# Kernel optimization log

Hardware: AMD Instinct MI355X
Metric: run time of the kernel (lower is better)

## Reference

```python
import jax, jax.numpy as jnp
import numpy as np

B, N, C, H, W = 4, 5, 64, 96, 288
DOWNSAMPLE_RATE = 4
DISCRETE_RATIO = 0.4
DECAY_WEIGHTS = jax.nn.softmax(jnp.array([1.0, 0.5], dtype=jnp.float32))  # frame=1, decay=0.5


def _warp_one(img, theta):
    # img: (C,H,W), theta: (2,3). Matches F.affine_grid + F.grid_sample
    # (bilinear, zeros padding, align_corners=True).
    c, h, w = img.shape
    xs = jnp.linspace(-1.0, 1.0, w, dtype=img.dtype)
    ys = jnp.linspace(-1.0, 1.0, h, dtype=img.dtype)
    gy, gx = jnp.meshgrid(ys, xs, indexing='ij')
    base = jnp.stack([gx.ravel(), gy.ravel(), jnp.ones(h * w, img.dtype)], 0)  # (3, HW)
    g = theta @ base  # (2, HW) normalized coords
    px = (g[0] + 1.0) * 0.5 * (w - 1)
    py = (g[1] + 1.0) * 0.5 * (h - 1)
    x0 = jnp.floor(px); y0 = jnp.floor(py)
    wx = px - x0; wy = py - y0
    def tap(yy, xx):
        yi = jnp.clip(yy, 0, h - 1).astype(jnp.int32)
        xi = jnp.clip(xx, 0, w - 1).astype(jnp.int32)
        valid = ((yy >= 0) & (yy <= h - 1) & (xx >= 0) & (xx <= w - 1)).astype(img.dtype)
        return img[:, yi, xi] * valid  # (C, HW)
    out = (tap(y0, x0) * (1 - wx) * (1 - wy)
           + tap(y0, x0 + 1) * wx * (1 - wy)
           + tap(y0 + 1, x0) * (1 - wx) * wy
           + tap(y0 + 1, x0 + 1) * wx * wy)
    return out.reshape(c, h, w)


def _frame_score(hist, mlp_w, mlp_b):
    # hist: (B,N,C,H,W) -> per-pixel ego-vs-neighbor attention score (B,N,1,H,W).
    b, n, c, h, w = hist.shape
    node = hist.reshape(b, n, c, h * w).transpose(0, 3, 1, 2)  # (B, P, N, C)
    ego = node[:, :, 0]          # (B, P, C)
    neigh = node[:, :, 1:]       # (B, P, N-1, C)
    # Query rows are all the repeated ego vector -> one row suffices (identical math).
    s = jnp.einsum('bpc,bpkc->bpk', ego, neigh) / jnp.sqrt(jnp.asarray(c, hist.dtype))
    attn = jax.nn.softmax(s, axis=-1)
    ctx = jnp.einsum('bpk,bpkc->bpc', attn, neigh)
    sc = jax.nn.sigmoid(ctx @ mlp_w.T + mlp_b)                   # (B, P, 1)
    sc = jnp.broadcast_to(sc[:, :, None, :], (b, h * w, n - 1, 1))
    ego_sc = jnp.ones((b, h * w, 1, 1), hist.dtype)
    overall = jnp.concatenate([ego_sc, sc], axis=2)              # (B, P, N, 1)
    return overall.transpose(0, 2, 3, 1).reshape(b, n, 1, h, w)


def _forward(x0, x1, pairwise_t_matrix, mlp_w, mlp_b):
    x0g = x0.reshape(B, N, C, H, W)
    x1g = x1.reshape(B, N, C, H, W)

    # --- TemporalSampling: weighted per-frame scores, threshold, 3x3 max-pool ---
    conf = DECAY_WEIGHTS[0] * _frame_score(x0g, mlp_w, mlp_b) \
         + DECAY_WEIGHTS[1] * _frame_score(x1g, mlp_w, mlp_b)      # (B,N,1,H,W)
    mask = jnp.where(conf > 0.5, jnp.float32(1.0), jnp.float32(0.0))
    mask = jax.lax.reduce_window(mask, -jnp.inf, jax.lax.max,
                                 (1, 1, 1, 3, 3), (1, 1, 1, 1, 1), 'SAME')
    x = x0g * mask  # broadcast over C

    # --- normalize pairwise transform to 2x3 affine matrices ---
    t = pairwise_t_matrix[:, :, :, jnp.array([0, 1])][:, :, :, :, jnp.array([0, 1, 3])]  # (B,L,L,2,3)
    t = t.at[..., 0, 1].mul(H / W)
    t = t.at[..., 1, 0].mul(W / H)
    t = t.at[..., 0, 2].set(t[..., 0, 2] / (DOWNSAMPLE_RATE * DISCRETE_RATIO * W) * 2)
    t = t.at[..., 1, 2].set(t[..., 1, 2] / (DOWNSAMPLE_RATE * DISCRETE_RATIO * H) * 2)
    theta = t[:, 0]  # (B,N,2,3): warp each cav into ego frame

    # --- per-agent warp ---
    warped = jax.vmap(jax.vmap(_warp_one))(x, theta)  # (B,N,C,H,W)

    # --- AttenFusion: per-pixel NxN attention, keep ego row ---
    nf = warped.reshape(B, N, C, H * W).transpose(0, 3, 1, 2)  # (B, P, N, C)
    s = jnp.einsum('bpc,bpkc->bpk', nf[:, :, 0], nf) / jnp.sqrt(jnp.asarray(C, nf.dtype))
    attn = jax.nn.softmax(s, axis=-1)
    ctx = jnp.einsum('bpk,bpkc->bpc', attn, nf)                 # (B, P, C)
    x_fuse = ctx.transpose(0, 2, 1).reshape(B, C, H, W)
    return x_fuse


def setup_inputs() -> dict:
    key = jax.random.key(0)
    k0, k1, k2, k3 = jax.random.split(key, 4)
    x0 = jax.random.normal(k0, (B * N, C, H, W), dtype=jnp.float32)
    x1 = jax.random.normal(k1, (B * N, C, H, W), dtype=jnp.float32)
    eye = jnp.broadcast_to(jnp.eye(4, dtype=jnp.float32), (B, N, N, 4, 4))
    pairwise_t_matrix = eye + 0.01 * jax.random.normal(k2, (B, N, N, 4, 4), dtype=jnp.float32)
    mlp_w = 0.1 * jax.random.normal(k3, (1, C), dtype=jnp.float32)
    mlp_b = jnp.zeros((1,), dtype=jnp.float32)
    record_len = jnp.full((B,), N, dtype=jnp.int32)
    return {"x0": x0, "x1": x1, "pairwise_t_matrix": pairwise_t_matrix,
            "mlp_w": mlp_w, "mlp_b": mlp_b, "record_len": record_len}


def reference(x0, x1, pairwise_t_matrix, mlp_w, mlp_b, record_len):
    # record_len is uniform (=N) and only determines the static regrouping.
    return _forward(x0, x1, pairwise_t_matrix, mlp_w, mlp_b)
```

## Files before the change

kernel.cpp:

```cpp
#include <hip/hip_runtime.h>
#include <cmath>

#define BB 4
#define NN 5
#define CC 64
#define HH 96
#define WW 288
#define PP (HH*WW)
#define BP (BB*PP)
#define CP (CC*PP)
#define NCP (NN*CC*PP)


static __device__ __forceinline__ float sigmoidf_(float x) {
    return 1.0f / (1.0f + expf(-x));
}

static __device__ __forceinline__ void tap_setup(
    int b, int h, int w, const float* __restrict__ pmat,
    const float* __restrict__ pooled, int offs[NN][4], float wts[NN][4])
{
    float gx = -1.0f + 2.0f * (float)w / (float)(WW - 1);
    float gy = -1.0f + 2.0f * (float)h / (float)(HH - 1);
    #pragma unroll
    for (int n = 0; n < NN; n++) {
        const float* m = pmat + ((size_t)(b * NN + 0) * NN + n) * 16;
        float t00 = m[0];
        float t01 = m[1] * ((float)HH / (float)WW);
        float t02 = m[3] * (float)(2.0 / (4.0 * 0.4 * (double)WW));
        float t10 = m[4] * ((float)WW / (float)HH);
        float t11 = m[5];
        float t12 = m[7] * (float)(2.0 / (4.0 * 0.4 * (double)HH));

        float g0 = t00 * gx + t01 * gy + t02;
        float g1 = t10 * gx + t11 * gy + t12;
        float px = (g0 + 1.0f) * 0.5f * (float)(WW - 1);
        float py = (g1 + 1.0f) * 0.5f * (float)(HH - 1);
        float x0f = floorf(px), y0f = floorf(py);
        float wx = px - x0f, wy = py - y0f;
        float bw[4] = { (1.f - wx) * (1.f - wy), wx * (1.f - wy),
                        (1.f - wx) * wy,         wx * wy };
        #pragma unroll
        for (int t = 0; t < 4; t++) {
            float xx = (t & 1) ? (x0f + 1.0f) : x0f;
            float yy = (t >> 1) ? (y0f + 1.0f) : y0f;
            int xi = min(max((int)xx, 0), WW - 1);
            int yi = min(max((int)yy, 0), HH - 1);
            float valid = (yy >= 0.0f && yy <= (float)(HH - 1) &&
                           xx >= 0.0f && xx <= (float)(WW - 1)) ? 1.0f : 0.0f;
            float mk = (n == 0) ? 1.0f : pooled[b * PP + yi * WW + xi];
            offs[n][t] = yi * WW + xi;
            wts[n][t]  = bw[t] * valid * mk;
        }
    }
}

__global__ __launch_bounds__(256) void mask_part_kernel(
    const float* __restrict__ x0, const float* __restrict__ x1,
    const float* __restrict__ mlp_w, float* __restrict__ mpart)
{
    int idx = blockIdx.x * blockDim.x + threadIdx.x;
    int seg = blockIdx.y;
    int b = idx / PP;
    int p = idx - b * PP;
    const float* xt = (seg >> 2) ? x1 : x0;
    int c0 = (seg & 3) * 16;
    const float* base = xt + (size_t)b * NCP + p;

    float d0=0.f,d1=0.f,d2=0.f,d3=0.f, m0=0.f,m1=0.f,m2=0.f,m3=0.f;
    #pragma unroll 4
    for (int ci = 0; ci < 16; ci++) {
        int c = c0 + ci;
        const float* q = base + (size_t)c * PP;
        float e  = q[0];
        float wc = mlp_w[c];
        float v1 = q[(size_t)1 * CP];
        float v2 = q[(size_t)2 * CP];
        float v3 = q[(size_t)3 * CP];
        float v4 = q[(size_t)4 * CP];
        d0 += e * v1;  m0 += wc * v1;
        d1 += e * v2;  m1 += wc * v2;
        d2 += e * v3;  m2 += wc * v3;
        d3 += e * v4;  m3 += wc * v4;
    }
    float vals[8] = {d0,d1,d2,d3,m0,m1,m2,m3};
    #pragma unroll
    for (int j = 0; j < 8; j++)
        mpart[((size_t)seg * 8 + j) * BP + idx] = vals[j];
}

__global__ __launch_bounds__(256) void mask_comb_kernel(
    const float* __restrict__ mpart, const float* __restrict__ mlp_b,
    float* __restrict__ premask)
{
    int idx = blockIdx.x * blockDim.x + threadIdx.x;
    float bias = mlp_b[0];
    float scv[2];
    #pragma unroll
    for (int t = 0; t < 2; t++) {
        float d[4] = {0.f,0.f,0.f,0.f};
        float m[4] = {0.f,0.f,0.f,0.f};
        #pragma unroll
        for (int cs = 0; cs < 4; cs++) {
            int seg = t * 4 + cs;
            #pragma unroll
            for (int j = 0; j < 4; j++) {
                d[j] += mpart[((size_t)seg * 8 + j) * BP + idx];
                m[j] += mpart[((size_t)seg * 8 + 4 + j) * BP + idx];
            }
        }
        float s0 = d[0]*0.125f, s1 = d[1]*0.125f, s2 = d[2]*0.125f, s3 = d[3]*0.125f;
        float mx = fmaxf(fmaxf(s0, s1), fmaxf(s2, s3));
        float e0 = expf(s0-mx), e1 = expf(s1-mx), e2 = expf(s2-mx), e3 = expf(s3-mx);
        float inv = 1.0f / (e0+e1+e2+e3);
        float z = (e0*m[0] + e1*m[1] + e2*m[2] + e3*m[3]) * inv + bias;
        scv[t] = sigmoidf_(z);
    }
    const float W0 = 0.6224593312018546f, W1 = 0.3775406687981454f;
    float conf = W0 * scv[0] + W1 * scv[1];
    premask[idx] = (conf > 0.5f) ? 1.0f : 0.0f;
}

__global__ __launch_bounds__(256) void pool_kernel(
    const float* __restrict__ pre, float* __restrict__ pooled)
{
    int idx = blockIdx.x * blockDim.x + threadIdx.x;
    int b = idx / PP;
    int p = idx - b * PP;
    int h = p / WW;
    int w = p - h * WW;
    const float* pb = pre + (size_t)b * PP;
    float m = 0.0f;
    #pragma unroll
    for (int dy = -1; dy <= 1; dy++) {
        int y = h + dy;
        if (y < 0 || y >= HH) continue;
        #pragma unroll
        for (int dx = -1; dx <= 1; dx++) {
            int x = w + dx;
            if (x < 0 || x >= WW) continue;
            m = fmaxf(m, pb[y * WW + x]);
        }
    }
    pooled[idx] = m;
}

__global__ __launch_bounds__(256) void dot_part_kernel(
    const float* __restrict__ x0, const float* __restrict__ pmat,
    const float* __restrict__ pooled, float* __restrict__ dpart)
{
    int idx = blockIdx.x * blockDim.x + threadIdx.x;
    int seg = blockIdx.y;
    int b = idx / PP;
    int p = idx - b * PP;
    int h = p / WW;
    int w = p - h * WW;

    int offs[NN][4];
    float wts[NN][4];
    tap_setup(b, h, w, pmat, pooled, offs, wts);

    const float* base = x0 + (size_t)b * NCP;
    float dot[NN] = {0.f,0.f,0.f,0.f,0.f};
    #pragma unroll 4
    for (int ci = 0; ci < 16; ci++) {
        int c = seg * 16 + ci;
        float v[NN];
        #pragma unroll
        for (int n = 0; n < NN; n++) {
            const float* pl = base + ((size_t)n * CC + c) * PP;
            float acc = 0.f;
            #pragma unroll
            for (int t = 0; t < 4; t++)
                acc += wts[n][t] * pl[offs[n][t]];
            v[n] = acc;
        }
        #pragma unroll
        for (int n = 0; n < NN; n++)
            dot[n] += v[0] * v[n];
    }
    #pragma unroll
    for (int n = 0; n < NN; n++)
        dpart[((size_t)n * 4 + seg) * BP + idx] = dot[n];
}

__global__ __launch_bounds__(256) void attn_kernel(
    const float* __restrict__ dpart, const float* __restrict__ pmat,
    const float* __restrict__ pooled, float* __restrict__ aw,
    int* __restrict__ offout)
{
    int idx = blockIdx.x * blockDim.x + threadIdx.x;
    int b = idx / PP;
    int p = idx - b * PP;
    int h = p / WW;
    int w = p - h * WW;

    float dot[NN];
    #pragma unroll
    for (int n = 0; n < NN; n++) {
        float s = 0.f;
        #pragma unroll
        for (int seg = 0; seg < 4; seg++)
            s += dpart[((size_t)n * 4 + seg) * BP + idx];
        dot[n] = s;
    }
    float s[NN], attn[NN];
    float mx = -INFINITY;
    #pragma unroll
    for (int n = 0; n < NN; n++) { s[n] = dot[n] * 0.125f; mx = fmaxf(mx, s[n]); }
    float sum = 0.f;
    #pragma unroll
    for (int n = 0; n < NN; n++) { attn[n] = expf(s[n] - mx); sum += attn[n]; }
    float inv = 1.0f / sum;

    int offs[NN][4];
    float wts[NN][4];
    tap_setup(b, h, w, pmat, pooled, offs, wts);
    #pragma unroll
    for (int n = 0; n < NN; n++) {
        float a = attn[n] * inv;
        #pragma unroll
        for (int t = 0; t < 4; t++) {
            aw[((size_t)n * 4 + t) * BP + idx]     = a * wts[n][t];
            offout[((size_t)n * 4 + t) * BP + idx] = offs[n][t];
        }
    }
}

__global__ __launch_bounds__(256) void out_kernel(
    const float* __restrict__ x0, const float* __restrict__ aw,
    const int* __restrict__ offin, float* __restrict__ out)
{
    int idx = blockIdx.x * blockDim.x + threadIdx.x;
    int c0  = blockIdx.y * 4;
    int b = idx / PP;
    int p = idx - b * PP;

    float a[20];
    int   o[20];
    #pragma unroll
    for (int j = 0; j < 20; j++) {
        a[j] = aw[(size_t)j * BP + idx];
        o[j] = offin[(size_t)j * BP + idx];
    }

    const float* base = x0 + (size_t)b * NCP + (size_t)c0 * PP;
    float acc0 = 0.f, acc1 = 0.f, acc2 = 0.f, acc3 = 0.f;
    #pragma unroll
    for (int j = 0; j < 20; j++) {
        int n = j >> 2;
        const float* pl = base + (size_t)n * CP + o[j];
        float w = a[j];
        acc0 += w * pl[0];
        acc1 += w * pl[(size_t)1 * PP];
        acc2 += w * pl[(size_t)2 * PP];
        acc3 += w * pl[(size_t)3 * PP];
    }
    size_t ob = ((size_t)b * CC + c0) * PP + p;
    out[ob]                 = acc0;
    out[ob + (size_t)1*PP]  = acc1;
    out[ob + (size_t)2*PP]  = acc2;
    out[ob + (size_t)3*PP]  = acc3;
}

extern "C" void kernel_launch(void* const* d_in, const int* in_sizes, int n_in,
                              void* d_out, int out_size, void* d_ws, size_t ws_size,
                              hipStream_t stream) {
    const float* x0    = (const float*)d_in[0];
    float*       x1    = (float*)d_in[1];
    const float* pmat  = (const float*)d_in[2];
    const float* mlp_w = (const float*)d_in[3];
    const float* mlp_b = (const float*)d_in[4];
    float* out = (float*)d_out;

    float* mpart  = out;
    float* s_pre  = x1;
    float* s_pool = x1 + (size_t)1  * BP;
    float* s_dot  = x1 + (size_t)2  * BP;
    float* s_aw   = x1 + (size_t)22 * BP;
    int*   s_off  = (int*)(x1 + (size_t)42 * BP);

    dim3 blk(256);
    dim3 g1(BP / 256, 8);
    dim3 g2(BP / 256);
    dim3 gf1(BP / 256, 4);
    dim3 gf2(BP / 256, 16);

    mask_part_kernel<<<g1,  blk, 0, stream>>>(x0, x1, mlp_w, mpart);
    mask_comb_kernel<<<g2,  blk, 0, stream>>>(mpart, mlp_b, s_pre);
    pool_kernel     <<<g2,  blk, 0, stream>>>(s_pre, s_pool);
    dot_part_kernel <<<gf1, blk, 0, stream>>>(x0, pmat, s_pool, s_dot);
    attn_kernel     <<<g2,  blk, 0, stream>>>(s_dot, pmat, s_pool, s_aw, s_off);
    out_kernel      <<<gf2, blk, 0, stream>>>(x0, s_aw, s_off, out);
}
```

Before: 474.4 us.

## Materialize warped features once and vectorize all kernels with float4

Adds a warp kernel that computes the bilinear-sampled neighbor features once and stores them. The dot-product and output kernels then read this warped tensor with coalesced float4 loads, so they no longer redo the 20-tap gathers or read per-tap weight and offset arrays. All per-pixel kernels now handle four pixels per thread using float4. The cost is an extra full-size write and two reads of the warped tensor, and the input buffers x0 and x1 are now overwritten as scratch space.

```diff
diff --git a/kernel.cpp b/kernel.cpp
--- a/kernel.cpp
+++ b/kernel.cpp
@@ -10,34 +10,177 @@
 #define BP (BB*PP)
 #define CP (CC*PP)
 #define NCP (NN*CC*PP)
+#define QP (PP/4)
+#define BQ (BP/4)
+#define CPQ (CP/4)
+#define NCPQ (NCP/4)
 
 
 static __device__ __forceinline__ float sigmoidf_(float x) {
     return 1.0f / (1.0f + expf(-x));
 }
-
-static __device__ __forceinline__ void tap_setup(
-    int b, int h, int w, const float* __restrict__ pmat,
-    const float* __restrict__ pooled, int offs[NN][4], float wts[NN][4])
-{
-    float gx = -1.0f + 2.0f * (float)w / (float)(WW - 1);
+static __device__ __forceinline__ float4 f4zero() {
+    return make_float4(0.f, 0.f, 0.f, 0.f);
+}
+static __device__ __forceinline__ void fma4(float4& a, float s, const float4& v) {
+    a.x += s * v.x; a.y += s * v.y; a.z += s * v.z; a.w += s * v.w;
+}
+static __device__ __forceinline__ void fma44(float4& a, const float4& s, const float4& v) {
+    a.x += s.x * v.x; a.y += s.y * v.y; a.z += s.z * v.z; a.w += s.w * v.w;
+}
+
+static __device__ __forceinline__ void theta_load(
+    const float* __restrict__ pmat, int b, int n,
+    float& t00, float& t01, float& t02, float& t10, float& t11, float& t12)
+{
+    const float* m = pmat + ((size_t)(b * NN + 0) * NN + n) * 16;
+    t00 = m[0];
+    t01 = m[1] * ((float)HH / (float)WW);
+    t02 = m[3] * (float)(2.0 / (4.0 * 0.4 * (double)WW));
+    t10 = m[4] * ((float)WW / (float)HH);
+    t11 = m[5];
+    t12 = m[7] * (float)(2.0 / (4.0 * 0.4 * (double)HH));
+}
+
+__global__ __launch_bounds__(256) void mask_part_kernel(
+    const float4* __restrict__ x0, const float4* __restrict__ x1,
+    const float* __restrict__ mlp_w, float4* __restrict__ mpart)
+{
+    int q   = blockIdx.x * 256 + threadIdx.x;
+    int seg = blockIdx.y;
+    int b  = q / QP;
+    int qp = q - b * QP;
+    const float4* xt = (seg >= 4) ? x1 : x0;
+    int c0 = (seg & 3) * 16;
+    const float4* base = xt + (size_t)b * NCPQ + qp;
+
+    float4 d0 = f4zero(), d1 = f4zero(), d2 = f4zero(), d3 = f4zero();
+    float4 m0 = f4zero(), m1 = f4zero(), m2 = f4zero(), m3 = f4zero();
+    #pragma unroll 4
+    for (int ci = 0; ci < 16; ci++) {
+        int c = c0 + ci;
+        const float4* qq = base + (size_t)c * QP;
+        float4 e  = qq[0];
+        float  wc = mlp_w[c];
+        float4 v1 = qq[(size_t)1 * CPQ];
+        float4 v2 = qq[(size_t)2 * CPQ];
+        float4 v3 = qq[(size_t)3 * CPQ];
+        float4 v4 = qq[(size_t)4 * CPQ];
+        fma44(d0, e, v1);  fma4(m0, wc, v1);
+        fma44(d1, e, v2);  fma4(m1, wc, v2);
+        fma44(d2, e, v3);  fma4(m2, wc, v3);
+        fma44(d3, e, v4);  fma4(m3, wc, v4);
+    }
+    float4 vals[8] = {d0, d1, d2, d3, m0, m1, m2, m3};
+    #pragma unroll
+    for (int j = 0; j < 8; j++)
+        mpart[((size_t)seg * 8 + j) * BQ + q] = vals[j];
+}
+
+__global__ __launch_bounds__(256) void mask_comb_kernel(
+    const float4* mpart, const float* mlp_b, float4* premask)
+{
+    int q = blockIdx.x * 256 + threadIdx.x;
+    float bias = mlp_b[0];
+    float4 scv[2];
+    #pragma unroll
+    for (int t = 0; t < 2; t++) {
+        float4 d[4] = {f4zero(), f4zero(), f4zero(), f4zero()};
+        float4 m[4] = {f4zero(), f4zero(), f4zero(), f4zero()};
+        #pragma unroll
+        for (int cs = 0; cs < 4; cs++) {
+            int seg = t * 4 + cs;
+            #pragma unroll
+            for (int j = 0; j < 4; j++) {
+                float4 dv = mpart[((size_t)seg * 8 + j) * BQ + q];
+                float4 mv = mpart[((size_t)seg * 8 + 4 + j) * BQ + q];
+                d[j].x += dv.x; d[j].y += dv.y; d[j].z += dv.z; d[j].w += dv.w;
+                m[j].x += mv.x; m[j].y += mv.y; m[j].z += mv.z; m[j].w += mv.w;
+            }
+        }
+        float out_c[4];
+        #pragma unroll
+        for (int k = 0; k < 4; k++) {
+            float dd[4] = { ((const float*)&d[0])[k], ((const float*)&d[1])[k],
+                            ((const float*)&d[2])[k], ((const float*)&d[3])[k] };
+            float mm[4] = { ((const float*)&m[0])[k], ((const float*)&m[1])[k],
+                            ((const float*)&m[2])[k], ((const float*)&m[3])[k] };
+            float s0 = dd[0]*0.125f, s1 = dd[1]*0.125f, s2 = dd[2]*0.125f, s3 = dd[3]*0.125f;
+            float mx = fmaxf(fmaxf(s0, s1), fmaxf(s2, s3));
+            float e0 = expf(s0-mx), e1 = expf(s1-mx), e2 = expf(s2-mx), e3 = expf(s3-mx);
+            float inv = 1.0f / (e0+e1+e2+e3);
+            float z = (e0*mm[0] + e1*mm[1] + e2*mm[2] + e3*mm[3]) * inv + bias;
+            out_c[k] = sigmoidf_(z);
+        }
+        scv[t] = make_float4(out_c[0], out_c[1], out_c[2], out_c[3]);
+    }
+    const float W0 = 0.6224593312018546f, W1 = 0.3775406687981454f;
+    float4 r;
+    r.x = (W0*scv[0].x + W1*scv[1].x > 0.5f) ? 1.f : 0.f;
+    r.y = (W0*scv[0].y + W1*scv[1].y > 0.5f) ? 1.f : 0.f;
+    r.z = (W0*scv[0].z + W1*scv[1].z > 0.5f) ? 1.f : 0.f;
+    r.w = (W0*scv[0].w + W1*scv[1].w > 0.5f) ? 1.f : 0.f;
+    premask[q] = r;
+}
+
+__global__ __launch_bounds__(256) void pool_kernel(
+    const float* __restrict__ pre, float4* __restrict__ pooled)
+{
+    int q  = blockIdx.x * 256 + threadIdx.x;
+    int b  = q / QP;
+    int qp = q - b * QP;
+    int p0 = qp * 4;
+    int h  = p0 / WW;
+    int w0 = p0 - h * WW;
+    const float* pb = pre + (size_t)b * PP;
+    float m[4] = {0.f, 0.f, 0.f, 0.f};
+    #pragma unroll
+    for (int dy = -1; dy <= 1; dy++) {
+        int y = h + dy;
+        if (y < 0 || y >= HH) continue;
+        const float* row = pb + y * WW;
+        float c_[6];
+        float4 mid = *(const float4*)(row + w0);
+        c_[0] = (w0 > 0) ? row[w0 - 1] : 0.f;
+        c_[1] = mid.x; c_[2] = mid.y; c_[3] = mid.z; c_[4] = mid.w;
+        c_[5] = (w0 + 4 < WW) ? row[w0 + 4] : 0.f;
+        #pragma unroll
+        for (int j = 0; j < 4; j++)
+            m[j] = fmaxf(m[j], fmaxf(c_[j], fmaxf(c_[j+1], c_[j+2])));
+    }
+    pooled[q] = make_float4(m[0], m[1], m[2], m[3]);
+}
+
+__global__ __launch_bounds__(256) void warp_kernel(
+    const float* __restrict__ x0, const float* __restrict__ pmat,
+    const float* __restrict__ pooled, float4* __restrict__ warped)
+{
+    int q    = blockIdx.x * 256 + threadIdx.x;
+    int n    = blockIdx.y >> 2;
+    int cseg = blockIdx.y & 3;
+    int c0   = cseg * 16;
+    int b  = q / QP;
+    int qp = q - b * QP;
+    int p0 = qp * 4;
+    int h  = p0 / WW;
+    int w0 = p0 - h * WW;
+
+    float t00, t01, t02, t10, t11, t12;
+    theta_load(pmat, b, n, t00, t01, t02, t10, t11, t12);
     float gy = -1.0f + 2.0f * (float)h / (float)(HH - 1);
-    #pragma unroll
-    for (int n = 0; n < NN; n++) {
-        const float* m = pmat + ((size_t)(b * NN + 0) * NN + n) * 16;
-        float t00 = m[0];
-        float t01 = m[1] * ((float)HH / (float)WW);
-        float t02 = m[3] * (float)(2.0 / (4.0 * 0.4 * (double)WW));
-        float t10 = m[4] * ((float)WW / (float)HH);
-        float t11 = m[5];
-        float t12 = m[7] * (float)(2.0 / (4.0 * 0.4 * (double)HH));
-
+
+    int   offs[4][4];
+    float wts [4][4];
+    const float* poolb = pooled + (size_t)b * PP;
+    #pragma unroll
+    for (int px = 0; px < 4; px++) {
+        float gx = -1.0f + 2.0f * (float)(w0 + px) / (float)(WW - 1);
         float g0 = t00 * gx + t01 * gy + t02;
         float g1 = t10 * gx + t11 * gy + t12;
-        float px = (g0 + 1.0f) * 0.5f * (float)(WW - 1);
-        float py = (g1 + 1.0f) * 0.5f * (float)(HH - 1);
-        float x0f = floorf(px), y0f = floorf(py);
-        float wx = px - x0f, wy = py - y0f;
+        float fx = (g0 + 1.0f) * 0.5f * (float)(WW - 1);
+        float fy = (g1 + 1.0f) * 0.5f * (float)(HH - 1);
+        float x0f = floorf(fx), y0f = floorf(fy);
+        float wx = fx - x0f, wy = fy - y0f;
         float bw[4] = { (1.f - wx) * (1.f - wy), wx * (1.f - wy),
                         (1.f - wx) * wy,         wx * wy };
         #pragma unroll
@@ -48,248 +191,156 @@
             int yi = min(max((int)yy, 0), HH - 1);
             float valid = (yy >= 0.0f && yy <= (float)(HH - 1) &&
                            xx >= 0.0f && xx <= (float)(WW - 1)) ? 1.0f : 0.0f;
-            float mk = (n == 0) ? 1.0f : pooled[b * PP + yi * WW + xi];
-            offs[n][t] = yi * WW + xi;
-            wts[n][t]  = bw[t] * valid * mk;
-        }
-    }
-}
-
-__global__ __launch_bounds__(256) void mask_part_kernel(
-    const float* __restrict__ x0, const float* __restrict__ x1,
-    const float* __restrict__ mlp_w, float* __restrict__ mpart)
-{
-    int idx = blockIdx.x * blockDim.x + threadIdx.x;
-    int seg = blockIdx.y;
-    int b = idx / PP;
-    int p = idx - b * PP;
-    const float* xt = (seg >> 2) ? x1 : x0;
-    int c0 = (seg & 3) * 16;
-    const float* base = xt + (size_t)b * NCP + p;
-
-    float d0=0.f,d1=0.f,d2=0.f,d3=0.f, m0=0.f,m1=0.f,m2=0.f,m3=0.f;
-    #pragma unroll 4
+            int off = yi * WW + xi;
+            float mk = (n == 0) ? 1.0f : poolb[off];
+            offs[px][t] = off;
+            wts [px][t] = bw[t] * valid * mk;
+        }
+    }
+
+    const float* src0 = x0 + ((size_t)(b * NN + n) * CC + c0) * PP;
+    float4* dst = warped + ((size_t)(b * NN + n) * CC + c0) * QP + qp;
+    #pragma unroll 2
     for (int ci = 0; ci < 16; ci++) {
-        int c = c0 + ci;
-        const float* q = base + (size_t)c * PP;
-        float e  = q[0];
-        float wc = mlp_w[c];
-        float v1 = q[(size_t)1 * CP];
-        float v2 = q[(size_t)2 * CP];
-        float v3 = q[(size_t)3 * CP];
-        float v4 = q[(size_t)4 * CP];
-        d0 += e * v1;  m0 += wc * v1;
-        d1 += e * v2;  m1 += wc * v2;
-        d2 += e * v3;  m2 += wc * v3;
-        d3 += e * v4;  m3 += wc * v4;
-    }
-    float vals[8] = {d0,d1,d2,d3,m0,m1,m2,m3};
-    #pragma unroll
-    for (int j = 0; j < 8; j++)
-        mpart[((size_t)seg * 8 + j) * BP + idx] = vals[j];
-}
-
-__global__ __launch_bounds__(256) void mask_comb_kernel(
-    const float* __restrict__ mpart, const float* __restrict__ mlp_b,
-    float* __restrict__ premask)
-{
-    int idx = blockIdx.x * blockDim.x + threadIdx.x;
-    float bias = mlp_b[0];
-    float scv[2];
-    #pragma unroll
-    for (int t = 0; t < 2; t++) {
-        float d[4] = {0.f,0.f,0.f,0.f};
-        float m[4] = {0.f,0.f,0.f,0.f};
-        #pragma unroll
-        for (int cs = 0; cs < 4; cs++) {
-            int seg = t * 4 + cs;
-            #pragma unroll
-            for (int j = 0; j < 4; j++) {
-                d[j] += mpart[((size_t)seg * 8 + j) * BP + idx];
-                m[j] += mpart[((size_t)seg * 8 + 4 + j) * BP + idx];
-            }
-        }
-        float s0 = d[0]*0.125f, s1 = d[1]*0.125f, s2 = d[2]*0.125f, s3 = d[3]*0.125f;
-        float mx = fmaxf(fmaxf(s0, s1), fmaxf(s2, s3));
-        float e0 = expf(s0-mx), e1 = expf(s1-mx), e2 = expf(s2-mx), e3 = expf(s3-mx);
-        float inv = 1.0f / (e0+e1+e2+e3);
-        float z = (e0*m[0] + e1*m[1] + e2*m[2] + e3*m[3]) * inv + bias;
-        scv[t] = sigmoidf_(z);
-    }
-    const float W0 = 0.6224593312018546f, W1 = 0.3775406687981454f;
-    float conf = W0 * scv[0] + W1 * scv[1];
-    premask[idx] = (conf > 0.5f) ? 1.0f : 0.0f;
-}
-
-__global__ __launch_bounds__(256) void pool_kernel(
-    const float* __restrict__ pre, float* __restrict__ pooled)
-{
-    int idx = blockIdx.x * blockDim.x + threadIdx.x;
-    int b = idx / PP;
-    int p = idx - b * PP;
-    int h = p / WW;
-    int w = p - h * WW;
-    const float* pb = pre + (size_t)b * PP;
-    float m = 0.0f;
-    #pragma unroll
-    for (int dy = -1; dy <= 1; dy++) {
-        int y = h + dy;
-        if (y < 0 || y >= HH) continue;
-        #pragma unroll
-        for (int dx = -1; dx <= 1; dx++) {
-            int x = w + dx;
-            if (x < 0 || x >= WW) continue;
-            m = fmaxf(m, pb[y * WW + x]);
-        }
-    }
-    pooled[idx] = m;
-}
-
-__global__ __launch_bounds__(256) void dot_part_kernel(
-    const float* __restrict__ x0, const float* __restrict__ pmat,
-    const float* __restrict__ pooled, float* __restrict__ dpart)
-{
-    int idx = blockIdx.x * blockDim.x + threadIdx.x;
-    int seg = blockIdx.y;
-    int b = idx / PP;
-    int p = idx - b * PP;
-    int h = p / WW;
-    int w = p - h * WW;
-
-    int offs[NN][4];
-    float wts[NN][4];
-    tap_setup(b, h, w, pmat, pooled, offs, wts);
-
-    const float* base = x0 + (size_t)b * NCP;
-    float dot[NN] = {0.f,0.f,0.f,0.f,0.f};
-    #pragma unroll 4
-    for (int ci = 0; ci < 16; ci++) {
-        int c = seg * 16 + ci;
-        float v[NN];
-        #pragma unroll
-        for (int n = 0; n < NN; n++) {
-            const float* pl = base + ((size_t)n * CC + c) * PP;
+        const float* bc = src0 + (size_t)ci * PP;
+        float o[4];
+        #pragma unroll
+        for (int px = 0; px < 4; px++) {
             float acc = 0.f;
             #pragma unroll
             for (int t = 0; t < 4; t++)
-                acc += wts[n][t] * pl[offs[n][t]];
-            v[n] = acc;
-        }
-        #pragma unroll
-        for (int n = 0; n < NN; n++)
-            dot[n] += v[0] * v[n];
+                acc += wts[px][t] * bc[offs[px][t]];
+            o[px] = acc;
+        }
+        dst[(size_t)ci * QP] = make_float4(o[0], o[1], o[2], o[3]);
+    }
+}
+
+__global__ __launch_bounds__(256) void dot_part_kernel(
+    const float4* __restrict__ warped, float4* __restrict__ dpart)
+{
+    int q    = blockIdx.x * 256 + threadIdx.x;
+    int cseg = blockIdx.y;
+    int b  = q / QP;
+    int qp = q - b * QP;
+    const float4* wv = warped + (size_t)b * NCPQ + qp;
+
+    float4 dot[NN] = {f4zero(), f4zero(), f4zero(), f4zero(), f4zero()};
+    #pragma unroll 4
+    for (int ci = 0; ci < 16; ci++) {
+        int c = cseg * 16 + ci;
+        float4 v0 = wv[(size_t)(0 * CC + c) * QP];
+        fma44(dot[0], v0, v0);
+        #pragma unroll
+        for (int n = 1; n < NN; n++) {
+            float4 vn = wv[(size_t)(n * CC + c) * QP];
+            fma44(dot[n], v0, vn);
+        }
     }
     #pragma unroll
     for (int n = 0; n < NN; n++)
-        dpart[((size_t)n * 4 + seg) * BP + idx] = dot[n];
+        dpart[((size_t)n * 4 + cseg) * BQ + q] = dot[n];
 }
 
 __global__ __launch_bounds__(256) void attn_kernel(
-    const float* __restrict__ dpart, const float* __restrict__ pmat,
-    const float* __restrict__ pooled, float* __restrict__ aw,
-    int* __restrict__ offout)
-{
-    int idx = blockIdx.x * blockDim.x + threadIdx.x;
-    int b = idx / PP;
-    int p = idx - b * PP;
-    int h = p / WW;
-    int w = p - h * WW;
-
-    float dot[NN];
+    const float4* __restrict__ dpart, float4* __restrict__ attn_out)
+{
+    int q = blockIdx.x * 256 + threadIdx.x;
+    float4 dot[NN];
     #pragma unroll
     for (int n = 0; n < NN; n++) {
-        float s = 0.f;
-        #pragma unroll
-        for (int seg = 0; seg < 4; seg++)
-            s += dpart[((size_t)n * 4 + seg) * BP + idx];
+        float4 s = f4zero();
+        #pragma unroll
+        for (int cs = 0; cs < 4; cs++) {
+            float4 v = dpart[((size_t)n * 4 + cs) * BQ + q];
+            s.x += v.x; s.y += v.y; s.z += v.z; s.w += v.w;
+        }
         dot[n] = s;
     }
-    float s[NN], attn[NN];
-    float mx = -INFINITY;
-    #pragma unroll
-    for (int n = 0; n < NN; n++) { s[n] = dot[n] * 0.125f; mx = fmaxf(mx, s[n]); }
-    float sum = 0.f;
-    #pragma unroll
-    for (int n = 0; n < NN; n++) { attn[n] = expf(s[n] - mx); sum += attn[n]; }
-    float inv = 1.0f / sum;
-
-    int offs[NN][4];
-    float wts[NN][4];
-    tap_setup(b, h, w, pmat, pooled, offs, wts);
-    #pragma unroll
-    for (int n = 0; n < NN; n++) {
-        float a = attn[n] * inv;
-        #pragma unroll
-        for (int t = 0; t < 4; t++) {
-            aw[((size_t)n * 4 + t) * BP + idx]     = a * wts[n][t];
-            offout[((size_t)n * 4 + t) * BP + idx] = offs[n][t];
-        }
-    }
+    float4 attn[NN];
+    #pragma unroll
+    for (int k = 0; k < 4; k++) {
+        float s[NN];
+        float mx = -INFINITY;
+        #pragma unroll
+        for (int n = 0; n < NN; n++) {
+            s[n] = ((const float*)&dot[n])[k] * 0.125f;
+            mx = fmaxf(mx, s[n]);
+        }
+        float sum = 0.f, e[NN];
+        #pragma unroll
+        for (int n = 0; n < NN; n++) { e[n] = expf(s[n] - mx); sum += e[n]; }
+        float inv = 1.0f / sum;
+        #pragma unroll
+        for (int n = 0; n < NN; n++) ((float*)&attn[n])[k] = e[n] * inv;
+    }
+    #pragma unroll
+    for (int n = 0; n < NN; n++)
+        attn_out[(size_t)n * BQ + q] = attn[n];
 }
 
 __global__ __launch_bounds__(256) void out_kernel(
-    const float* __restrict__ x0, const float* __restrict__ aw,
-    const int* __restrict__ offin, float* __restrict__ out)
-{
-    int idx = blockIdx.x * blockDim.x + threadIdx.x;
-    int c0  = blockIdx.y * 4;
-    int b = idx / PP;
-    int p = idx - b * PP;
-
-    float a[20];
-    int   o[20];
-    #pragma unroll
-    for (int j = 0; j < 20; j++) {
-        a[j] = aw[(size_t)j * BP + idx];
-        o[j] = offin[(size_t)j * BP + idx];
-    }
-
-    const float* base = x0 + (size_t)b * NCP + (size_t)c0 * PP;
-    float acc0 = 0.f, acc1 = 0.f, acc2 = 0.f, acc3 = 0.f;
-    #pragma unroll
-    for (int j = 0; j < 20; j++) {
-        int n = j >> 2;
-        const float* pl = base + (size_t)n * CP + o[j];
-        float w = a[j];
-        acc0 += w * pl[0];
-        acc1 += w * pl[(size_t)1 * PP];
-        acc2 += w * pl[(size_t)2 * PP];
-        acc3 += w * pl[(size_t)3 * PP];
-    }
-    size_t ob = ((size_t)b * CC + c0) * PP + p;
-    out[ob]                 = acc0;
-    out[ob + (size_t)1*PP]  = acc1;
-    out[ob + (size_t)2*PP]  = acc2;
-    out[ob + (size_t)3*PP]  = acc3;
+    const float4* __restrict__ warped, const float4* __restrict__ attn,
+    float4* __restrict__ out)
+{
+    int q  = blockIdx.x * 256 + threadIdx.x;
+    int c0 = blockIdx.y * 4;
+    int b  = q / QP;
+    int qp = q - b * QP;
+
+    float4 a[NN];
+    #pragma unroll
+    for (int n = 0; n < NN; n++)
+        a[n] = attn[(size_t)n * BQ + q];
+
+    const float4* wv = warped + (size_t)b * NCPQ + qp;
+    #pragma unroll
+    for (int ci = 0; ci < 4; ci++) {
+        int c = c0 + ci;
+        float4 acc = f4zero();
+        #pragma unroll
+        for (int n = 0; n < NN; n++) {
+            float4 v = wv[(size_t)(n * CC + c) * QP];
+            fma44(acc, a[n], v);
+        }
+        out[((size_t)b * CC + c) * QP + qp] = acc;
+    }
 }
 
 extern "C" void kernel_launch(void* const* d_in, const int* in_sizes, int n_in,
                               void* d_out, int out_size, void* d_ws, size_t ws_size,
                               hipStream_t stream) {
-    const float* x0    = (const float*)d_in[0];
+    float*       x0    = (float*)d_in[0];
     float*       x1    = (float*)d_in[1];
     const float* pmat  = (const float*)d_in[2];
     const float* mlp_w = (const float*)d_in[3];
     const float* mlp_b = (const float*)d_in[4];
     float* out = (float*)d_out;
 
-    float* mpart  = out;
-    float* s_pre  = x1;
-    float* s_pool = x1 + (size_t)1  * BP;
-    float* s_dot  = x1 + (size_t)2  * BP;
-    float* s_aw   = x1 + (size_t)22 * BP;
-    int*   s_off  = (int*)(x1 + (size_t)42 * BP);
+    float4* x0_4     = (float4*)x0;
+    float4* x1_4     = (float4*)x1;
+    float4* out_4    = (float4*)out;
+    float4* mpart    = out_4;
+    float*  pre_s    = out;
+    float4* pre_4    = out_4;
+    float*  pool_s   = out + (size_t)BP;
+    float4* pool_4   = out_4 + (size_t)BQ;
+    float4* dpart    = out_4 + (size_t)2 * BQ;
+    float4* warped   = x1_4;
+    float4* attn_s   = x0_4;
 
     dim3 blk(256);
-    dim3 g1(BP / 256, 8);
-    dim3 g2(BP / 256);
-    dim3 gf1(BP / 256, 4);
-    dim3 gf2(BP / 256, 16);
-
-    mask_part_kernel<<<g1,  blk, 0, stream>>>(x0, x1, mlp_w, mpart);
-    mask_comb_kernel<<<g2,  blk, 0, stream>>>(mpart, mlp_b, s_pre);
-    pool_kernel     <<<g2,  blk, 0, stream>>>(s_pre, s_pool);
-    dot_part_kernel <<<gf1, blk, 0, stream>>>(x0, pmat, s_pool, s_dot);
-    attn_kernel     <<<g2,  blk, 0, stream>>>(s_dot, pmat, s_pool, s_aw, s_off);
-    out_kernel      <<<gf2, blk, 0, stream>>>(x0, s_aw, s_off, out);
-}
+    dim3 gA1(BQ / 256, 8);
+    dim3 gS (BQ / 256);
+    dim3 gW (BQ / 256, 20);
+    dim3 gD (BQ / 256, 4);
+    dim3 gO (BQ / 256, 16);
+
+    mask_part_kernel<<<gA1, blk, 0, stream>>>(x0_4, x1_4, mlp_w, mpart);
+    mask_comb_kernel<<<gS,  blk, 0, stream>>>(mpart, mlp_b, pre_4);
+    pool_kernel     <<<gS,  blk, 0, stream>>>(pre_s, pool_4);
+    warp_kernel     <<<gW,  blk, 0, stream>>>(x0, pmat, pool_s, warped);
+    dot_part_kernel <<<gD,  blk, 0, stream>>>(warped, dpart);
+    attn_kernel     <<<gS,  blk, 0, stream>>>(dpart, attn_s);
+    out_kernel      <<<gO,  blk, 0, stream>>>(warped, attn_s, out_4);
+}
```

Measured after the change: 553.7 us. 16.7% more time.
